# Kernel optimization log

Hardware: AMD Instinct MI355X
Metric: run time of the kernel (lower is better)

Reference implementation:

```python
import jax, jax.numpy as jnp
import numpy as np

N, E, D_IN, D_H, N_CLASSES = 50000, 800000, 128, 128, 40
D_OUT = D_H // 2
LN_EPS = 1e-5


def _seg_mean(msgs, dst, n_nodes):
    # mean aggregation over incoming edges; isolated nodes get 0 (like PyG mean)
    s = jax.ops.segment_sum(msgs, dst, num_segments=n_nodes)
    cnt = jax.ops.segment_sum(jnp.ones((dst.shape[0], 1), msgs.dtype), dst, num_segments=n_nodes)
    return s / jnp.maximum(cnt, 1.0)


def _sage(x, src, dst, Wl, bl, Wr):
    # PyG SAGEConv(mean): lin_l(mean_j x_j) + lin_r(x_i); lin_l has bias, lin_r none
    agg = _seg_mean(x[src], dst, x.shape[0])  # [N, d_in]
    return agg @ Wl + bl + x @ Wr


def _layernorm(x, g, b):
    mu = jnp.mean(x, axis=-1, keepdims=True)
    var = jnp.mean(jnp.square(x - mu), axis=-1, keepdims=True)
    return (x - mu) * jax.lax.rsqrt(var + LN_EPS) * g + b


def setup_inputs() -> dict:
    key = jax.random.key(0)
    ks = jax.random.split(key, 20)
    sc = lambda d: 1.0 / np.sqrt(d)
    inp = {
        "x": jax.random.normal(ks[0], (N, D_IN), dtype=jnp.float32),
        "edge_index": jax.random.randint(ks[1], (2, E), 0, N, dtype=jnp.int32),
        # block1 (in==hidden -> proj is Identity)
        "Wl1": jax.random.normal(ks[2], (D_IN, D_H), jnp.float32) * sc(D_IN),
        "bl1": jnp.zeros((D_H,), jnp.float32),
        "Wr1": jax.random.normal(ks[3], (D_IN, D_H), jnp.float32) * sc(D_IN),
        "g1": jnp.ones((D_H,), jnp.float32),
        "b1": jnp.zeros((D_H,), jnp.float32),
        # block2
        "Wl2": jax.random.normal(ks[4], (D_H, D_H), jnp.float32) * sc(D_H),
        "bl2": jnp.zeros((D_H,), jnp.float32),
        "Wr2": jax.random.normal(ks[5], (D_H, D_H), jnp.float32) * sc(D_H),
        "g2": jnp.ones((D_H,), jnp.float32),
        "b2": jnp.zeros((D_H,), jnp.float32),
        # conv_out: hidden -> hidden//2
        "Wl3": jax.random.normal(ks[6], (D_H, D_OUT), jnp.float32) * sc(D_H),
        "bl3": jnp.zeros((D_OUT,), jnp.float32),
        "Wr3": jax.random.normal(ks[7], (D_H, D_OUT), jnp.float32) * sc(D_H),
        # classifier: LayerNorm(D_OUT) + Linear(D_OUT, n_classes)
        "gc": jnp.ones((D_OUT,), jnp.float32),
        "bc": jnp.zeros((D_OUT,), jnp.float32),
        "Wc": jax.random.normal(ks[8], (D_OUT, N_CLASSES), jnp.float32) * sc(D_OUT),
        "bcls": jnp.zeros((N_CLASSES,), jnp.float32),
    }
    return inp


def reference(x, edge_index, Wl1, bl1, Wr1, g1, b1, Wl2, bl2, Wr2, g2, b2,
              Wl3, bl3, Wr3, gc, bc, Wc, bcls):
    src, dst = edge_index[0], edge_index[1]
    # block1: SAGE -> LN -> GELU -> (dropout eval=identity) -> +x (proj=Identity)
    h = _sage(x, src, dst, Wl1, bl1, Wr1)
    x = jax.nn.gelu(_layernorm(h, g1, b1), approximate=False) + x
    # block2
    h = _sage(x, src, dst, Wl2, bl2, Wr2)
    x = jax.nn.gelu(_layernorm(h, g2, b2), approximate=False) + x
    # conv_out + GELU
    x = jax.nn.gelu(_sage(x, src, dst, Wl3, bl3, Wr3), approximate=False)
    # classifier: LN then Linear
    return _layernorm(x, gc, bc) @ Wc + bcls
```

## Files before the change

kernel.cpp:

```cpp
#include <hip/hip_runtime.h>
#include <math.h>


typedef __attribute__((ext_vector_type(8))) short bf16x8;
typedef __attribute__((ext_vector_type(4))) float f32x4;

#define NWG 256
#define NBK 196
#define CAP2 6144

__device__ inline float gelu_f(float x) {
    float u = x * (1.0f + 0.044715f * x * x);
    return x / (1.0f + __expf(-1.5957691216057308f * u));
}

__device__ inline ushort f2b(float f) {
    uint u = __float_as_uint(f);
    u += 0x7fffu + ((u >> 16) & 1u);
    return (ushort)(u >> 16);
}

__device__ inline float b2f(ushort h) { return __uint_as_float((uint)h << 16); }


__global__ __launch_bounds__(256) void k_hist(const int* __restrict__ dst, int e,
                                              int* __restrict__ cnts) {
    __shared__ int h[NBK];
    const int tid = threadIdx.x;
    const int wg = blockIdx.x;
    for (int i = tid; i < NBK; i += 256) h[i] = 0;
    __syncthreads();
    const int ch = (e + NWG - 1) / NWG;
    const int lo = wg * ch;
    const int hi = min(e, lo + ch);
    for (int i = lo + tid; i < hi; i += 256) atomicAdd(&h[dst[i] >> 8], 1);
    __syncthreads();
    for (int i = tid; i < NBK; i += 256) cnts[i * NWG + wg] = h[i];
}

__global__ __launch_bounds__(256) void k_scanP1(const int* __restrict__ in,
                                                int* __restrict__ out,
                                                int* __restrict__ part, int m) {
    __shared__ int sm[256];
    const int tid = threadIdx.x;
    const int base = blockIdx.x * 1024 + tid * 4;
    int4 v = make_int4(0, 0, 0, 0);
    if (base + 3 < m) {
        v = *(const int4*)(in + base);
    } else {
        if (base + 0 < m) v.x = in[base + 0];
        if (base + 1 < m) v.y = in[base + 1];
        if (base + 2 < m) v.z = in[base + 2];
        if (base + 3 < m) v.w = in[base + 3];
    }
    int s = v.x + v.y + v.z + v.w;
    sm[tid] = s;
    __syncthreads();
#pragma unroll
    for (int d = 1; d < 256; d <<= 1) {
        int add = (tid >= d) ? sm[tid - d] : 0;
        __syncthreads();
        sm[tid] += add;
        __syncthreads();
    }
    int ex = (tid ? sm[tid - 1] : 0);
    if (base + 0 < m) out[base + 0] = ex;
    ex += v.x;
    if (base + 1 < m) out[base + 1] = ex;
    ex += v.y;
    if (base + 2 < m) out[base + 2] = ex;
    ex += v.z;
    if (base + 3 < m) out[base + 3] = ex;
    if (tid == 255) part[blockIdx.x] = sm[255];
}

__global__ __launch_bounds__(256) void k_scanP2(int* __restrict__ out,
                                                const int* __restrict__ part, int m) {
    const int tid = threadIdx.x;
    const int bid = blockIdx.x;
    const int lane = tid & 63;
    int s = 0;
    for (int j = lane; j < bid; j += 64) s += part[j];
#pragma unroll
    for (int d = 32; d > 0; d >>= 1) s += __shfl_xor(s, d);
    const int i0 = bid * 1024 + tid * 4;
#pragma unroll
    for (int j = 0; j < 4; ++j) {
        int i = i0 + j;
        if (i < m) out[i] += s;
    }
}

__global__ __launch_bounds__(256) void k_scat(const int* __restrict__ src,
                                              const int* __restrict__ dst, int e,
                                              const int* __restrict__ bases,
                                              uint* __restrict__ pairs) {
    __shared__ int cur[NBK];
    const int tid = threadIdx.x;
    const int wg = blockIdx.x;
    for (int i = tid; i < NBK; i += 256) cur[i] = bases[i * NWG + wg];
    __syncthreads();
    const int ch = (e + NWG - 1) / NWG;
    const int lo = wg * ch;
    const int hi = min(e, lo + ch);
    for (int i = lo + tid; i < hi; i += 256) {
        int d = dst[i];
        int pos = atomicAdd(&cur[d >> 8], 1);
        pairs[pos] = (uint)src[i] | ((uint)(d & 255) << 16);
    }
}

__global__ __launch_bounds__(256) void k_sortC(const uint* __restrict__ pairs,
                                               const int* __restrict__ bases, int e,
                                               int* __restrict__ csr, int* __restrict__ off,
                                               int* __restrict__ cntout, int n) {
    __shared__ int hist[256];
    __shared__ int curl[256];
    __shared__ int sm[256];
    __shared__ int buf[CAP2];
    const int bk = blockIdx.x;
    const int tid = threadIdx.x;
    const int start = bases[bk * NWG];
    const int end = (bk == NBK - 1) ? e : bases[(bk + 1) * NWG];
    int m = end - start;
    if (m > CAP2) m = CAP2;

    hist[tid] = 0;
    __syncthreads();
    for (int i = tid; i < m; i += 256) atomicAdd(&hist[(pairs[start + i] >> 16) & 255], 1);
    __syncthreads();
    int v = hist[tid];
    sm[tid] = v;
    __syncthreads();
#pragma unroll
    for (int d = 1; d < 256; d <<= 1) {
        int add = (tid >= d) ? sm[tid - d] : 0;
        __syncthreads();
        sm[tid] += add;
        __syncthreads();
    }
    int excl = sm[tid] - v;
    int node = (bk << 8) + tid;
    if (node < n) {
        off[node] = start + excl;
        cntout[node] = v;
    }
    curl[tid] = excl;
    __syncthreads();
    for (int i = tid; i < m; i += 256) {
        uint w = pairs[start + i];
        int pos = atomicAdd(&curl[(w >> 16) & 255], 1);
        buf[pos] = (int)(w & 0xffffu);
    }
    __syncthreads();
    for (int i = tid; i < m; i += 256) csr[start + i] = buf[i];
}


__global__ void k_cast(const float* __restrict__ in, ushort* __restrict__ out, int nvec4) {
    int t = blockIdx.x * blockDim.x + threadIdx.x;
    int stride = gridDim.x * blockDim.x;
    for (int i = t; i < nvec4; i += stride) {
        float4 v = ((const float4*)in)[i];
        ushort4 o;
        o.x = f2b(v.x);
        o.y = f2b(v.y);
        o.z = f2b(v.z);
        o.w = f2b(v.w);
        ((ushort4*)out)[i] = o;
    }
}

__global__ void k_wprep(const float* __restrict__ Wl, const float* __restrict__ Wr,
                        int KH, int C, ushort* __restrict__ Wt) {
    int t = blockIdx.x * blockDim.x + threadIdx.x;
    int total = C * 2 * KH;
    if (t >= total) return;
    int c = t / (2 * KH), k = t % (2 * KH);
    float v = (k < KH) ? Wl[(size_t)k * C + c] : Wr[(size_t)(k - KH) * C + c];
    Wt[t] = f2b(v);
}

__global__ void k_wprepC(const float* __restrict__ Wc, ushort* __restrict__ Wct) {
    int t = blockIdx.x * blockDim.x + threadIdx.x;
    if (t >= 64 * 64) return;
    int c = t >> 6, k = t & 63;
    float v = (c < 40) ? Wc[k * 40 + c] : 0.f;
    Wct[t] = f2b(v);
}


__global__ __launch_bounds__(256) void k_agg(const ushort* __restrict__ X,
                                             const int* __restrict__ off,
                                             const int* __restrict__ cnt,
                                             const int* __restrict__ csr,
                                             ushort* __restrict__ agg, int n) {
    const int wave = threadIdx.x >> 6;
    const int lane = threadIdx.x & 63;
    const int base = blockIdx.x * 32 + wave * 8;
#pragma unroll 1
    for (int j = 0; j < 8; ++j) {
        const int i = base + j;
        if (i >= n) return;
        int s0 = off[i];
        int deg = cnt[i];
        int c = 0;
        if (lane < deg) c = csr[s0 + lane];
        float a0 = 0.f, a1 = 0.f;
        const int dcap = deg < 64 ? deg : 64;
        int t = 0;
        for (; t + 3 < dcap; t += 4) {
            int i0 = __shfl(c, t), i1 = __shfl(c, t + 1);
            int i2 = __shfl(c, t + 2), i3 = __shfl(c, t + 3);
            uint u0 = *((const uint*)(X + (size_t)i0 * 128) + lane);
            uint u1 = *((const uint*)(X + (size_t)i1 * 128) + lane);
            uint u2 = *((const uint*)(X + (size_t)i2 * 128) + lane);
            uint u3 = *((const uint*)(X + (size_t)i3 * 128) + lane);
            a0 += __uint_as_float(u0 << 16) + __uint_as_float(u1 << 16) +
                  __uint_as_float(u2 << 16) + __uint_as_float(u3 << 16);
            a1 += __uint_as_float(u0 & 0xffff0000u) + __uint_as_float(u1 & 0xffff0000u) +
                  __uint_as_float(u2 & 0xffff0000u) + __uint_as_float(u3 & 0xffff0000u);
        }
        for (; t < dcap; ++t) {
            uint u0 = *((const uint*)(X + (size_t)__shfl(c, t) * 128) + lane);
            a0 += __uint_as_float(u0 << 16);
            a1 += __uint_as_float(u0 & 0xffff0000u);
        }
        for (int tt = s0 + 64; tt < s0 + deg; ++tt) {
            uint u0 = *((const uint*)(X + (size_t)csr[tt] * 128) + lane);
            a0 += __uint_as_float(u0 << 16);
            a1 += __uint_as_float(u0 & 0xffff0000u);
        }
        float inv = 1.0f / (float)(deg > 1 ? deg : 1);
        uint pk = (uint)f2b(a0 * inv) | ((uint)f2b(a1 * inv) << 16);
        *((uint*)(agg + (size_t)i * 128) + lane) = pk;
    }
}


template <int DOUT, int EPI>
__global__ __launch_bounds__(256) void k_gemm(
    const ushort* __restrict__ Agg, const ushort* __restrict__ Xb,
    const ushort* __restrict__ Wt, const float* __restrict__ bias,
    const float* __restrict__ g, const float* __restrict__ b,
    ushort* __restrict__ OutB, int n) {
    constexpr int CT = DOUT / 64;
    const int tid = threadIdx.x;
    const int wave = tid >> 6;
    const int lane = tid & 63;
    const int l16 = lane & 15;
    const int g4 = lane >> 4;
    const int row0 = blockIdx.x * 32;

    __shared__ __align__(16) ushort As[32 * 256];

    int colv[CT];
#pragma unroll
    for (int ct = 0; ct < CT; ++ct) colv[ct] = (wave * CT + ct) * 16 + l16;

    bf16x8 bfr[CT][8];
#pragma unroll
    for (int ct = 0; ct < CT; ++ct) {
        const ushort* wp = Wt + (size_t)colv[ct] * 256 + g4 * 8;
#pragma unroll
        for (int ks = 0; ks < 8; ++ks) bfr[ct][ks] = *(const bf16x8*)(wp + ks * 32);
    }

    {
        const int row = tid >> 3;
        const int jj = tid & 7;
        int gr = row0 + row;
        if (gr > n - 1) gr = n - 1;
        const ushort* pa = Agg + (size_t)gr * 128;
        const ushort* pb = Xb + (size_t)gr * 128;
        uint4 v0 = *(const uint4*)(pa + jj * 8);
        uint4 v1 = *(const uint4*)(pa + (jj + 8) * 8);
        uint4 v2 = *(const uint4*)(pb + jj * 8);
        uint4 v3 = *(const uint4*)(pb + (jj + 8) * 8);
        const int sw = (row & 7) << 4;
        char* lb = (char*)As + row * 512;
        *(uint4*)(lb + ((jj * 16) ^ sw)) = v0;
        *(uint4*)(lb + (((jj + 8) * 16) ^ sw)) = v1;
        *(uint4*)(lb + (((jj + 16) * 16) ^ sw)) = v2;
        *(uint4*)(lb + (((jj + 24) * 16) ^ sw)) = v3;
    }

    float biasv[CT], gv[CT], bbv[CT];
#pragma unroll
    for (int ct = 0; ct < CT; ++ct) {
        biasv[ct] = bias[colv[ct]];
        gv[ct] = g[colv[ct]];
        bbv[ct] = b[colv[ct]];
    }

    __syncthreads();

    f32x4 acc[2][CT];
#pragma unroll
    for (int rt = 0; rt < 2; ++rt)
#pragma unroll
        for (int ct = 0; ct < CT; ++ct) {
            acc[rt][ct][0] = 0.f;
            acc[rt][ct][1] = 0.f;
            acc[rt][ct][2] = 0.f;
            acc[rt][ct][3] = 0.f;
        }
#pragma unroll
    for (int ks = 0; ks < 8; ++ks) {
        bf16x8 a[2];
#pragma unroll
        for (int rt = 0; rt < 2; ++rt) {
            const int row = rt * 16 + l16;
            a[rt] = *(const bf16x8*)((const char*)As + row * 512 +
                                     ((ks * 64 + g4 * 16) ^ ((row & 7) << 4)));
        }
#pragma unroll
        for (int rt = 0; rt < 2; ++rt)
#pragma unroll
            for (int ct = 0; ct < CT; ++ct)
                acc[rt][ct] = __builtin_amdgcn_mfma_f32_16x16x32_bf16(a[rt], bfr[ct][ks],
                                                                     acc[rt][ct], 0, 0, 0);
    }

    __shared__ float sP[32][4];
    __shared__ float qP[32][4];
    float v[2][4][CT];
    float sv[2][4], qv[2][4];
#pragma unroll
    for (int rt = 0; rt < 2; ++rt)
#pragma unroll
        for (int reg = 0; reg < 4; ++reg) {
            float s = 0.f, q = 0.f;
#pragma unroll
            for (int ct = 0; ct < CT; ++ct) {
                float t = acc[rt][ct][reg] + biasv[ct];
                if (EPI == 3) t = gelu_f(t);
                v[rt][reg][ct] = t;
                s += t;
                q += t * t;
            }
            sv[rt][reg] = s;
            qv[rt][reg] = q;
        }
#pragma unroll
    for (int m = 1; m < 16; m <<= 1)
#pragma unroll
        for (int rt = 0; rt < 2; ++rt)
#pragma unroll
            for (int reg = 0; reg < 4; ++reg) {
                sv[rt][reg] += __shfl_xor(sv[rt][reg], m);
                qv[rt][reg] += __shfl_xor(qv[rt][reg], m);
            }
    if (l16 == 0) {
#pragma unroll
        for (int rt = 0; rt < 2; ++rt)
#pragma unroll
            for (int reg = 0; reg < 4; ++reg) {
                int rib = rt * 16 + g4 * 4 + reg;
                sP[rib][wave] = sv[rt][reg];
                qP[rib][wave] = qv[rt][reg];
            }
    }
    __syncthreads();
#pragma unroll
    for (int rt = 0; rt < 2; ++rt) {
#pragma unroll
        for (int reg = 0; reg < 4; ++reg) {
            int rib = rt * 16 + g4 * 4 + reg;
            float s = sP[rib][0] + sP[rib][1] + sP[rib][2] + sP[rib][3];
            float q = qP[rib][0] + qP[rib][1] + qP[rib][2] + qP[rib][3];
            float mu = s * (1.0f / (float)DOUT);
            float var = q * (1.0f / (float)DOUT) - mu * mu;
            float rs = rsqrtf(fmaxf(var, 0.f) + 1e-5f);
            int r = row0 + rib;
            if (r >= n) continue;
#pragma unroll
            for (int ct = 0; ct < CT; ++ct) {
                float y = (v[rt][reg][ct] - mu) * rs * gv[ct] + bbv[ct];
                if (EPI == 1) {
                    ushort rh = *(const ushort*)((const char*)As + rib * 512 +
                                                 ((256 + 2 * colv[ct]) ^ ((rib & 7) << 4)));
                    y = gelu_f(y) + b2f(rh);
                }
                OutB[(size_t)r * DOUT + colv[ct]] = f2b(y);
            }
        }
    }
}


__global__ __launch_bounds__(256) void k_mm(const ushort* __restrict__ Y,
                                            const ushort* __restrict__ Wct,
                                            const float* __restrict__ bcls,
                                            float* __restrict__ Out, int n) {
    const int tid = threadIdx.x;
    const int wave = tid >> 6;
    const int lane = tid & 63;
    const int l16 = lane & 15;
    const int g4 = lane >> 4;
    const int row0 = blockIdx.x * 32;
    const int col = wave * 16 + l16;

    bf16x8 bfr[2];
#pragma unroll
    for (int ks = 0; ks < 2; ++ks)
        bfr[ks] = *(const bf16x8*)(Wct + (size_t)col * 64 + ks * 32 + g4 * 8);

    f32x4 acc[2];
#pragma unroll
    for (int rt = 0; rt < 2; ++rt) {
        acc[rt][0] = 0.f;
        acc[rt][1] = 0.f;
        acc[rt][2] = 0.f;
        acc[rt][3] = 0.f;
    }

    int arow[2];
#pragma unroll
    for (int rt = 0; rt < 2; ++rt) {
        int r = row0 + rt * 16 + l16;
        arow[rt] = (r < n) ? r : (n - 1);
    }

#pragma unroll
    for (int ks = 0; ks < 2; ++ks)
#pragma unroll
        for (int rt = 0; rt < 2; ++rt) {
            bf16x8 a = *(const bf16x8*)(Y + (size_t)arow[rt] * 64 + ks * 32 + g4 * 8);
            acc[rt] = __builtin_amdgcn_mfma_f32_16x16x32_bf16(a, bfr[ks], acc[rt], 0, 0, 0);
        }

    const float bcv = (col < 40) ? bcls[col] : 0.f;
#pragma unroll
    for (int rt = 0; rt < 2; ++rt)
#pragma unroll
        for (int reg = 0; reg < 4; ++reg) {
            int r = row0 + rt * 16 + g4 * 4 + reg;
            if (r < n && col < 40) Out[(size_t)r * 40 + col] = acc[rt][reg] + bcv;
        }
}


extern "C" void kernel_launch(void* const* d_in, const int* in_sizes, int n_in,
                              void* d_out, int out_size, void* d_ws, size_t ws_size,
                              hipStream_t stream) {
    const float* x   = (const float*)d_in[0];
    const int* ei    = (const int*)d_in[1];
    const float* Wl1 = (const float*)d_in[2];
    const float* bl1 = (const float*)d_in[3];
    const float* Wr1 = (const float*)d_in[4];
    const float* g1  = (const float*)d_in[5];
    const float* b1  = (const float*)d_in[6];
    const float* Wl2 = (const float*)d_in[7];
    const float* bl2 = (const float*)d_in[8];
    const float* Wr2 = (const float*)d_in[9];
    const float* g2  = (const float*)d_in[10];
    const float* b2  = (const float*)d_in[11];
    const float* Wl3 = (const float*)d_in[12];
    const float* bl3 = (const float*)d_in[13];
    const float* Wr3 = (const float*)d_in[14];
    const float* gc  = (const float*)d_in[15];
    const float* bc  = (const float*)d_in[16];
    const float* Wc  = (const float*)d_in[17];
    const float* bcls= (const float*)d_in[18];

    const int n = in_sizes[0] / 128;
    const int e = in_sizes[1] / 2;
    const int* src = ei;
    const int* dst = ei + e;

    char* w = (char*)d_ws;
    size_t o = 0;
    auto alloc = [&](size_t bytes) -> char* {
        char* p = w + o;
        o = (o + bytes + 511) & ~(size_t)511;
        return p;
    };
    int* cnts    = (int*)alloc((size_t)NBK * NWG * 4);
    int* bases   = (int*)alloc((size_t)NBK * NWG * 4);
    int* part    = (int*)alloc(256 * 4);
    uint* pairs  = (uint*)alloc((size_t)e * 4);
    int* csr     = (int*)alloc((size_t)e * 4);
    int* off     = (int*)alloc((size_t)n * 4);
    int* cnt     = (int*)alloc((size_t)n * 4);
    ushort* xB   = (ushort*)alloc((size_t)n * 128 * 2);
    ushort* aggB = (ushort*)alloc((size_t)n * 128 * 2);
    ushort* xaB  = (ushort*)alloc((size_t)n * 128 * 2);
    ushort* xbB  = (ushort*)alloc((size_t)n * 128 * 2);
    ushort* yB   = (ushort*)alloc((size_t)n * 64 * 2);
    ushort* W1t  = (ushort*)alloc((size_t)128 * 256 * 2);
    ushort* W2t  = (ushort*)alloc((size_t)128 * 256 * 2);
    ushort* W3t  = (ushort*)alloc((size_t)64 * 256 * 2);
    ushort* Wct  = (ushort*)alloc((size_t)64 * 64 * 2);
    (void)ws_size;

    const int m = NBK * NWG;
    const int sblk = (m + 1023) / 1024;
    k_hist<<<NWG, 256, 0, stream>>>(dst, e, cnts);
    k_scanP1<<<sblk, 256, 0, stream>>>(cnts, bases, part, m);
    k_scanP2<<<sblk, 256, 0, stream>>>(bases, part, m);
    k_scat<<<NWG, 256, 0, stream>>>(src, dst, e, bases, pairs);
    k_sortC<<<NBK, 256, 0, stream>>>(pairs, bases, e, csr, off, cnt, n);

    k_cast<<<2048, 256, 0, stream>>>(x, xB, n * 128 / 4);
    k_wprep<<<(128 * 256 + 255) / 256, 256, 0, stream>>>(Wl1, Wr1, 128, 128, W1t);
    k_wprep<<<(128 * 256 + 255) / 256, 256, 0, stream>>>(Wl2, Wr2, 128, 128, W2t);
    k_wprep<<<(64 * 256 + 255) / 256, 256, 0, stream>>>(Wl3, Wr3, 128, 64, W3t);
    k_wprepC<<<16, 256, 0, stream>>>(Wc, Wct);

    const int gg = (n + 31) / 32;

    k_agg<<<gg, 256, 0, stream>>>(xB, off, cnt, csr, aggB, n);
    k_gemm<128, 1><<<gg, 256, 0, stream>>>(aggB, xB, W1t, bl1, g1, b1, xaB, n);
    k_agg<<<gg, 256, 0, stream>>>(xaB, off, cnt, csr, aggB, n);
    k_gemm<128, 1><<<gg, 256, 0, stream>>>(aggB, xaB, W2t, bl2, g2, b2, xbB, n);
    k_agg<<<gg, 256, 0, stream>>>(xbB, off, cnt, csr, aggB, n);
    k_gemm<64, 3><<<gg, 256, 0, stream>>>(aggB, xbB, W3t, bl3, gc, bc, yB, n);
    k_mm<<<gg, 256, 0, stream>>>(yB, Wct, bcls, (float*)d_out, n);
}
```

Baseline: 207.5 us.

## Transform-before-aggregate for conv_out and load GEMM tiles directly into LDS

For the third SAGE layer, the projection is applied before aggregation: x@[Wl3|Wr3] is computed first, and the 64-wide projected features are gathered and averaged. This halves the gather width for that layer, and bias, GELU and LayerNorm are fused into the aggregation kernel. Separately, the GEMM A-tile staging now uses global_load_lds direct-to-LDS loads instead of register round-trips. The change adds an extra kernel and intermediate buffers, and the order of the mean and the matmul now differs in bf16 rounding.

```diff
diff --git a/kernel.cpp b/kernel.cpp
--- a/kernel.cpp
+++ b/kernel.cpp
@@ -4,6 +4,9 @@
 
 typedef __attribute__((ext_vector_type(8))) short bf16x8;
 typedef __attribute__((ext_vector_type(4))) float f32x4;
+
+#define AS1 __attribute__((address_space(1)))
+#define AS3 __attribute__((address_space(3)))
 
 #define NWG 256
 #define NBK 196
@@ -12,6 +15,12 @@
 __device__ inline float gelu_f(float x) {
     float u = x * (1.0f + 0.044715f * x * x);
     return x / (1.0f + __expf(-1.5957691216057308f * u));
+}
+
+__device__ inline float wave_sum(float v) {
+#pragma unroll
+    for (int d = 32; d > 0; d >>= 1) v += __shfl_xor(v, d);
+    return v;
 }
 
 __device__ inline ushort f2b(float f) {
@@ -178,6 +187,15 @@
     if (t >= total) return;
     int c = t / (2 * KH), k = t % (2 * KH);
     float v = (k < KH) ? Wl[(size_t)k * C + c] : Wr[(size_t)(k - KH) * C + c];
+    Wt[t] = f2b(v);
+}
+
+__global__ void k_wprepW3(const float* __restrict__ Wl, const float* __restrict__ Wr,
+                          ushort* __restrict__ Wt) {
+    int t = blockIdx.x * blockDim.x + threadIdx.x;
+    if (t >= 128 * 128) return;
+    int c = t >> 7, k = t & 127;
+    float v = (c < 64) ? Wl[(size_t)k * 64 + c] : Wr[(size_t)k * 64 + (c - 64)];
     Wt[t] = f2b(v);
 }
 
@@ -238,13 +256,12 @@
 }
 
 
-template <int DOUT, int EPI>
 __global__ __launch_bounds__(256) void k_gemm(
     const ushort* __restrict__ Agg, const ushort* __restrict__ Xb,
     const ushort* __restrict__ Wt, const float* __restrict__ bias,
     const float* __restrict__ g, const float* __restrict__ b,
     ushort* __restrict__ OutB, int n) {
-    constexpr int CT = DOUT / 64;
+    constexpr int CT = 2;
     const int tid = threadIdx.x;
     const int wave = tid >> 6;
     const int lane = tid & 63;
@@ -253,6 +270,24 @@
     const int row0 = blockIdx.x * 32;
 
     __shared__ __align__(16) ushort As[32 * 256];
+    __shared__ float sP[32][4];
+    __shared__ float qP[32][4];
+
+    {
+        const int slot = lane & 31;
+#pragma unroll
+        for (int i = 0; i < 4; ++i) {
+            const int rr = (wave * 4 + i) * 2 + (lane >> 5);
+            int gr = row0 + rr;
+            if (gr > n - 1) gr = n - 1;
+            const int srcb = (slot * 16) ^ ((rr & 7) << 4);
+            const char* gp = (srcb < 256)
+                                 ? (const char*)Agg + (size_t)gr * 256 + srcb
+                                 : (const char*)Xb + (size_t)gr * 256 + (srcb - 256);
+            char* lp = (char*)As + (wave * 4 + i) * 1024;
+            __builtin_amdgcn_global_load_lds((const AS1 void*)gp, (AS3 void*)lp, 16, 0, 0);
+        }
+    }
 
     int colv[CT];
 #pragma unroll
@@ -265,26 +300,6 @@
 #pragma unroll
         for (int ks = 0; ks < 8; ++ks) bfr[ct][ks] = *(const bf16x8*)(wp + ks * 32);
     }
-
-    {
-        const int row = tid >> 3;
-        const int jj = tid & 7;
-        int gr = row0 + row;
-        if (gr > n - 1) gr = n - 1;
-        const ushort* pa = Agg + (size_t)gr * 128;
-        const ushort* pb = Xb + (size_t)gr * 128;
-        uint4 v0 = *(const uint4*)(pa + jj * 8);
-        uint4 v1 = *(const uint4*)(pa + (jj + 8) * 8);
-        uint4 v2 = *(const uint4*)(pb + jj * 8);
-        uint4 v3 = *(const uint4*)(pb + (jj + 8) * 8);
-        const int sw = (row & 7) << 4;
-        char* lb = (char*)As + row * 512;
-        *(uint4*)(lb + ((jj * 16) ^ sw)) = v0;
-        *(uint4*)(lb + (((jj + 8) * 16) ^ sw)) = v1;
-        *(uint4*)(lb + (((jj + 16) * 16) ^ sw)) = v2;
-        *(uint4*)(lb + (((jj + 24) * 16) ^ sw)) = v3;
-    }
-
     float biasv[CT], gv[CT], bbv[CT];
 #pragma unroll
     for (int ct = 0; ct < CT; ++ct) {
@@ -322,8 +337,6 @@
                                                                      acc[rt][ct], 0, 0, 0);
     }
 
-    __shared__ float sP[32][4];
-    __shared__ float qP[32][4];
     float v[2][4][CT];
     float sv[2][4], qv[2][4];
 #pragma unroll
@@ -333,11 +346,10 @@
             float s = 0.f, q = 0.f;
 #pragma unroll
             for (int ct = 0; ct < CT; ++ct) {
-                float t = acc[rt][ct][reg] + biasv[ct];
-                if (EPI == 3) t = gelu_f(t);
-                v[rt][reg][ct] = t;
-                s += t;
-                q += t * t;
+                float tv = acc[rt][ct][reg] + biasv[ct];
+                v[rt][reg][ct] = tv;
+                s += tv;
+                q += tv * tv;
             }
             sv[rt][reg] = s;
             qv[rt][reg] = q;
@@ -369,22 +381,154 @@
             int rib = rt * 16 + g4 * 4 + reg;
             float s = sP[rib][0] + sP[rib][1] + sP[rib][2] + sP[rib][3];
             float q = qP[rib][0] + qP[rib][1] + qP[rib][2] + qP[rib][3];
-            float mu = s * (1.0f / (float)DOUT);
-            float var = q * (1.0f / (float)DOUT) - mu * mu;
+            float mu = s * (1.0f / 128.0f);
+            float var = q * (1.0f / 128.0f) - mu * mu;
             float rs = rsqrtf(fmaxf(var, 0.f) + 1e-5f);
             int r = row0 + rib;
             if (r >= n) continue;
 #pragma unroll
             for (int ct = 0; ct < CT; ++ct) {
                 float y = (v[rt][reg][ct] - mu) * rs * gv[ct] + bbv[ct];
-                if (EPI == 1) {
-                    ushort rh = *(const ushort*)((const char*)As + rib * 512 +
-                                                 ((256 + 2 * colv[ct]) ^ ((rib & 7) << 4)));
-                    y = gelu_f(y) + b2f(rh);
-                }
-                OutB[(size_t)r * DOUT + colv[ct]] = f2b(y);
+                ushort rh = *(const ushort*)((const char*)As + rib * 512 +
+                                             ((256 + 2 * colv[ct]) ^ ((rib & 7) << 4)));
+                y = gelu_f(y) + b2f(rh);
+                OutB[(size_t)r * 128 + colv[ct]] = f2b(y);
             }
         }
+    }
+}
+
+
+__global__ __launch_bounds__(256) void k_gemmW3(const ushort* __restrict__ X,
+                                                const ushort* __restrict__ Wt,
+                                                ushort* __restrict__ Z,
+                                                ushort* __restrict__ Wo, int n) {
+    constexpr int CT = 2;
+    const int tid = threadIdx.x;
+    const int wave = tid >> 6;
+    const int lane = tid & 63;
+    const int l16 = lane & 15;
+    const int g4 = lane >> 4;
+    const int row0 = blockIdx.x * 32;
+
+    __shared__ __align__(16) ushort As[32 * 128];
+
+    {
+        const int slot = lane & 15;
+#pragma unroll
+        for (int i = 0; i < 2; ++i) {
+            const int rr = (wave * 2 + i) * 4 + (lane >> 4);
+            int gr = row0 + rr;
+            if (gr > n - 1) gr = n - 1;
+            const int srcb = (slot * 16) ^ ((rr & 7) << 4);
+            const char* gp = (const char*)X + (size_t)gr * 256 + srcb;
+            char* lp = (char*)As + (wave * 2 + i) * 1024;
+            __builtin_amdgcn_global_load_lds((const AS1 void*)gp, (AS3 void*)lp, 16, 0, 0);
+        }
+    }
+
+    int colv[CT];
+#pragma unroll
+    for (int ct = 0; ct < CT; ++ct) colv[ct] = (wave * CT + ct) * 16 + l16;
+
+    bf16x8 bfr[CT][4];
+#pragma unroll
+    for (int ct = 0; ct < CT; ++ct) {
+        const ushort* wp = Wt + (size_t)colv[ct] * 128 + g4 * 8;
+#pragma unroll
+        for (int ks = 0; ks < 4; ++ks) bfr[ct][ks] = *(const bf16x8*)(wp + ks * 32);
+    }
+
+    __syncthreads();
+
+    f32x4 acc[2][CT];
+#pragma unroll
+    for (int rt = 0; rt < 2; ++rt)
+#pragma unroll
+        for (int ct = 0; ct < CT; ++ct) {
+            acc[rt][ct][0] = 0.f;
+            acc[rt][ct][1] = 0.f;
+            acc[rt][ct][2] = 0.f;
+            acc[rt][ct][3] = 0.f;
+        }
+#pragma unroll
+    for (int ks = 0; ks < 4; ++ks) {
+        bf16x8 a[2];
+#pragma unroll
+        for (int rt = 0; rt < 2; ++rt) {
+            const int row = rt * 16 + l16;
+            a[rt] = *(const bf16x8*)((const char*)As + row * 256 +
+                                     ((ks * 64 + g4 * 16) ^ ((row & 7) << 4)));
+        }
+#pragma unroll
+        for (int rt = 0; rt < 2; ++rt)
+#pragma unroll
+            for (int ct = 0; ct < CT; ++ct)
+                acc[rt][ct] = __builtin_amdgcn_mfma_f32_16x16x32_bf16(a[rt], bfr[ct][ks],
+                                                                     acc[rt][ct], 0, 0, 0);
+    }
+
+#pragma unroll
+    for (int rt = 0; rt < 2; ++rt)
+#pragma unroll
+        for (int reg = 0; reg < 4; ++reg) {
+            int r = row0 + rt * 16 + g4 * 4 + reg;
+            if (r >= n) continue;
+#pragma unroll
+            for (int ct = 0; ct < CT; ++ct) {
+                int col = colv[ct];
+                ushort hv = f2b(acc[rt][ct][reg]);
+                if (col < 64)
+                    Z[(size_t)r * 64 + col] = hv;
+                else
+                    Wo[(size_t)r * 64 + (col - 64)] = hv;
+            }
+        }
+}
+
+
+__global__ __launch_bounds__(256) void k_aggpost3(
+    const ushort* __restrict__ Z3, const ushort* __restrict__ W3,
+    const int* __restrict__ off, const int* __restrict__ cnt,
+    const int* __restrict__ csr, const float* __restrict__ bl3,
+    const float* __restrict__ gc, const float* __restrict__ bc,
+    ushort* __restrict__ Yout, int n) {
+    const int wave = threadIdx.x >> 6;
+    const int lane = threadIdx.x & 63;
+    const int base = blockIdx.x * 32 + wave * 8;
+
+    const float blv = bl3[lane];
+    const float gv = gc[lane];
+    const float bv = bc[lane];
+
+#pragma unroll 1
+    for (int j = 0; j < 8; ++j) {
+        const int i = base + j;
+        if (i >= n) return;
+        int s0 = off[i];
+        int deg = cnt[i];
+        int c = 0;
+        if (lane < deg) c = csr[s0 + lane];
+        float a = 0.f;
+        const int dcap = deg < 64 ? deg : 64;
+        int t = 0;
+        for (; t + 3 < dcap; t += 4) {
+            int i0 = __shfl(c, t), i1 = __shfl(c, t + 1);
+            int i2 = __shfl(c, t + 2), i3 = __shfl(c, t + 3);
+            a += b2f(Z3[(size_t)i0 * 64 + lane]) + b2f(Z3[(size_t)i1 * 64 + lane]) +
+                 b2f(Z3[(size_t)i2 * 64 + lane]) + b2f(Z3[(size_t)i3 * 64 + lane]);
+        }
+        for (; t < dcap; ++t) a += b2f(Z3[(size_t)__shfl(c, t) * 64 + lane]);
+        for (int tt = s0 + 64; tt < s0 + deg; ++tt)
+            a += b2f(Z3[(size_t)csr[tt] * 64 + lane]);
+        float inv = 1.0f / (float)(deg > 1 ? deg : 1);
+        float h = a * inv + b2f(W3[(size_t)i * 64 + lane]) + blv;
+        float hg = gelu_f(h);
+        float mu = wave_sum(hg) * (1.0f / 64.0f);
+        float d = hg - mu;
+        float var = wave_sum(d * d) * (1.0f / 64.0f);
+        float y = d * rsqrtf(var + 1e-5f) * gv + bv;
+        Yout[(size_t)i * 64 + lane] = f2b(y);
     }
 }
 
@@ -487,10 +631,12 @@
     ushort* aggB = (ushort*)alloc((size_t)n * 128 * 2);
     ushort* xaB  = (ushort*)alloc((size_t)n * 128 * 2);
     ushort* xbB  = (ushort*)alloc((size_t)n * 128 * 2);
+    ushort* Zb   = (ushort*)alloc((size_t)n * 64 * 2);
+    ushort* Wb   = (ushort*)alloc((size_t)n * 64 * 2);
     ushort* yB   = (ushort*)alloc((size_t)n * 64 * 2);
     ushort* W1t  = (ushort*)alloc((size_t)128 * 256 * 2);
     ushort* W2t  = (ushort*)alloc((size_t)128 * 256 * 2);
-    ushort* W3t  = (ushort*)alloc((size_t)64 * 256 * 2);
+    ushort* W3c  = (ushort*)alloc((size_t)128 * 128 * 2);
     ushort* Wct  = (ushort*)alloc((size_t)64 * 64 * 2);
     (void)ws_size;
 
@@ -505,16 +651,16 @@
     k_cast<<<2048, 256, 0, stream>>>(x, xB, n * 128 / 4);
     k_wprep<<<(128 * 256 + 255) / 256, 256, 0, stream>>>(Wl1, Wr1, 128, 128, W1t);
     k_wprep<<<(128 * 256 + 255) / 256, 256, 0, stream>>>(Wl2, Wr2, 128, 128, W2t);
-    k_wprep<<<(64 * 256 + 255) / 256, 256, 0, stream>>>(Wl3, Wr3, 128, 64, W3t);
+    k_wprepW3<<<(128 * 128 + 255) / 256, 256, 0, stream>>>(Wl3, Wr3, W3c);
     k_wprepC<<<16, 256, 0, stream>>>(Wc, Wct);
 
     const int gg = (n + 31) / 32;
 
     k_agg<<<gg, 256, 0, stream>>>(xB, off, cnt, csr, aggB, n);
-    k_gemm<128, 1><<<gg, 256, 0, stream>>>(aggB, xB, W1t, bl1, g1, b1, xaB, n);
+    k_gemm<<<gg, 256, 0, stream>>>(aggB, xB, W1t, bl1, g1, b1, xaB, n);
     k_agg<<<gg, 256, 0, stream>>>(xaB, off, cnt, csr, aggB, n);
-    k_gemm<128, 1><<<gg, 256, 0, stream>>>(aggB, xaB, W2t, bl2, g2, b2, xbB, n);
-    k_agg<<<gg, 256, 0, stream>>>(xbB, off, cnt, csr, aggB, n);
-    k_gemm<64, 3><<<gg, 256, 0, stream>>>(aggB, xbB, W3t, bl3, gc, bc, yB, n);
+    k_gemm<<<gg, 256, 0, stream>>>(aggB, xaB, W2t, bl2, g2, b2, xbB, n);
+    k_gemmW3<<<gg, 256, 0, stream>>>(xbB, W3c, Zb, Wb, n);
+    k_aggpost3<<<gg, 256, 0, stream>>>(Zb, Wb, off, cnt, csr, bl3, gc, bc, yB, n);
     k_mm<<<gg, 256, 0, stream>>>(yB, Wct, bcls, (float*)d_out, n);
 }
```

New measurement: 207.4 us. No clear change (-0.0%).
